# Kernel optimization log

Measured on AMD Instinct MI355X. Metric: run time of the kernel, lower is better.

Reference implementation:

```python
import jax, jax.numpy as jnp
import numpy as np

EMBED = 512
HEADS = 8
HEAD_DIM = EMBED // HEADS


def setup_inputs() -> dict:
    key = jax.random.key(0)
    ks = jax.random.split(key, 9)
    N, L = 4, 2048
    values = jax.random.normal(ks[0], (N, L, EMBED), dtype=jnp.float32)
    keys = jax.random.normal(ks[1], (N, L, EMBED), dtype=jnp.float32)
    query = jax.random.normal(ks[2], (N, L, EMBED), dtype=jnp.float32)
    mask = jax.random.randint(ks[3], (N, 1, 1, L), 0, 2, dtype=jnp.int32)
    s_h = 1.0 / np.sqrt(HEAD_DIM).astype(np.float32)
    s_e = 1.0 / np.sqrt(EMBED).astype(np.float32)
    Wv = jax.random.normal(ks[4], (HEAD_DIM, HEAD_DIM), dtype=jnp.float32) * s_h
    Wk = jax.random.normal(ks[5], (HEAD_DIM, HEAD_DIM), dtype=jnp.float32) * s_h
    Wq = jax.random.normal(ks[6], (HEAD_DIM, HEAD_DIM), dtype=jnp.float32) * s_h
    Wo = jax.random.normal(ks[7], (EMBED, EMBED), dtype=jnp.float32) * s_e
    bo = jnp.zeros((EMBED,), dtype=jnp.float32)
    return {"values": values, "keys": keys, "query": query, "mask": mask,
            "Wv": Wv, "Wk": Wk, "Wq": Wq, "Wo": Wo, "bo": bo}


def reference(values, keys, query, mask, Wv, Wk, Wq, Wo, bo):
    N, Lq, E = query.shape
    D = Wv.shape[0]
    H = E // D
    Lk = keys.shape[1]
    # split heads: [N, L, H, D]
    v = values.reshape(N, values.shape[1], H, D)
    k = keys.reshape(N, Lk, H, D)
    q = query.reshape(N, Lq, H, D)
    # per-head linear projections (nn.Linear: x @ W^T, no bias)
    v = jnp.einsum("nlhd,ed->nlhe", v, Wv)
    k = jnp.einsum("nlhd,ed->nlhe", k, Wk)
    q = jnp.einsum("nlhd,ed->nlhe", q, Wq)
    # energy: [N, H, Lq, Lk]
    energy = jnp.einsum("nqhd,nkhd->nhqk", q, k)
    energy = jnp.where(mask == 0, jnp.float32(-1e20), energy)
    # NOTE: original scales by sqrt(embed_size), not sqrt(head_dim)
    attn = jax.nn.softmax(energy / jnp.sqrt(jnp.float32(E)), axis=3)
    out = jnp.einsum("nhqk,nkhd->nqhd", attn, v).reshape(N, Lq, E)
    return out @ Wo.T + bo
```

## Files before the change

### kernel.cpp

```cpp
#include <hip/hip_runtime.h>

#define LSEQ 2048
#define EMB  512
#define NH   8
#define HD   64
#define NBATCH 4
#define QSCALE (0.044194173824159216f * 1.4426950408889634f)

using short8  = __attribute__((ext_vector_type(8))) short;
using short4v = __attribute__((ext_vector_type(4))) short;
using f32x4   = __attribute__((ext_vector_type(4))) float;

__device__ __forceinline__ short bf16r(float f) {
  union { float f; unsigned u; } x; x.f = f;
  unsigned r = x.u + 0x7FFFu + ((x.u >> 16) & 1u);
  return (short)(r >> 16);
}

__device__ __forceinline__ float exp2v(float x) {
  float r;
  asm("v_exp_f32 %0, %1" : "=v"(r) : "v"(x));
  return r;
}

__device__ __forceinline__ unsigned cvtpk(float lo, float hi) {
  unsigned r;
  asm("v_cvt_pk_bf16_f32 %0, %1, %2" : "=v"(r) : "v"(lo), "v"(hi));
  return r;
}

__device__ __forceinline__ void stage16(const void* g, void* l) {
  __builtin_amdgcn_global_load_lds(
      (const __attribute__((address_space(1))) unsigned int*)g,
      (__attribute__((address_space(3))) unsigned int*)l, 16, 0, 0);
}

__device__ __forceinline__ short8 cvt8(const float* __restrict__ p) {
  float4 a = ((const float4*)p)[0];
  float4 b = ((const float4*)p)[1];
  short8 r;
  r[0]=bf16r(a.x); r[1]=bf16r(a.y); r[2]=bf16r(a.z); r[3]=bf16r(a.w);
  r[4]=bf16r(b.x); r[5]=bf16r(b.y); r[6]=bf16r(b.z); r[7]=bf16r(b.w);
  return r;
}

__device__ __forceinline__ short8 ld8(const short* __restrict__ p) {
  return *(const short8*)p;
}

__global__ __launch_bounds__(256) void prep_kernel(
    const int* __restrict__ mask, float* __restrict__ fbias,
    int* __restrict__ kidx, int* __restrict__ meta,
    const float* __restrict__ Wq, const float* __restrict__ Wk,
    const float* __restrict__ Wv, short* __restrict__ Wqb,
    short* __restrict__ Wkb, short* __restrict__ Wvb) {
  __shared__ int ssum[256];
  int b = blockIdx.x;
  int tid = threadIdx.x;
  if (b < 4) {
    int n = b;
    int base = n * LSEQ;
    int loc[8], c = 0;
#pragma unroll
    for (int j = 0; j < 8; j++) { loc[j] = mask[base + tid * 8 + j] != 0; c += loc[j]; }
    ssum[tid] = c;
    __syncthreads();
    for (int off = 1; off < 256; off <<= 1) {
      int v = (tid >= off) ? ssum[tid - off] : 0;
      __syncthreads();
      ssum[tid] += v;
      __syncthreads();
    }
    int total = ssum[255];
    int excl = ssum[tid] - c;
    int qz = (total == 0);
#pragma unroll
    for (int j = 0; j < 8; j++) {
      int i = tid * 8 + j;
      kidx[base + i] = qz ? i : 0;
      fbias[base + i] = (qz || i < total) ? 0.f : -1e30f;
    }
    __syncthreads();
    if (!qz) {
      int pos = excl;
#pragma unroll
      for (int j = 0; j < 8; j++)
        if (loc[j]) { kidx[base + pos] = tid * 8 + j; pos++; }
    }
    if (tid == 0) {
      meta[n] = qz ? (LSEQ / 64) : ((total + 63) >> 6);
      meta[4 + n] = qz;
    }
  } else {
    int t = (b - 4) >> 2;
    int i = ((b - 4) & 3) * 256 + tid;
    const float* W = (t == 0) ? Wq : (t == 1) ? Wk : Wv;
    short* O = (t == 0) ? Wqb : (t == 1) ? Wkb : Wvb;
    float sc = (t == 0) ? QSCALE : 1.f;
    float4 v = ((const float4*)W)[i];
    short4v r;
    r[0]=bf16r(v.x*sc); r[1]=bf16r(v.y*sc); r[2]=bf16r(v.z*sc); r[3]=bf16r(v.w*sc);
    ((short4v*)O)[i] = r;
  }
}

__global__ __launch_bounds__(256) void proj_kernel(
    const float* __restrict__ keys, const float* __restrict__ values,
    const short* __restrict__ Wkb, const short* __restrict__ Wvb,
    const int* __restrict__ kidx, const int* __restrict__ meta,
    short* __restrict__ Kp, short* __restrict__ Vt) {
  __shared__ short tile[64][72];
  int t = blockIdx.y + 1;
  const float* x = (t == 1) ? keys : values;
  const short* W = (t == 1) ? Wkb  : Wvb;
  int idx = blockIdx.x;
  int lt = idx & 31, h = (idx >> 5) & 7, n = idx >> 8;
  int tid = threadIdx.x, lane = tid & 63, w = tid >> 6;
  int row16 = lane & 15, g = lane >> 4;
  int lbase = lt * 64 + w * 16;

  if (lbase >= ((meta[n] + 1) & ~1) * 64) return;
  int gidx = kidx[n * LSEQ + lbase + row16];
  const float* xr = x + ((size_t)(n * LSEQ + gidx)) * EMB + h * HD + g * 8;
  short8 a0 = cvt8(xr);
  short8 a1 = cvt8(xr + 32);

  f32x4 acc[4];
#pragma unroll
  for (int et = 0; et < 4; et++) acc[et] = (f32x4){0.f, 0.f, 0.f, 0.f};
#pragma unroll
  for (int et = 0; et < 4; et++) {
    const short* wr = W + (size_t)(et * 16 + row16) * HD + g * 8;
    short8 b0 = ld8(wr);
    short8 b1 = ld8(wr + 32);
    acc[et] = __builtin_amdgcn_mfma_f32_16x16x32_bf16(a0, b0, acc[et], 0, 0, 0);
    acc[et] = __builtin_amdgcn_mfma_f32_16x16x32_bf16(a1, b1, acc[et], 0, 0, 0);
  }

  if (t == 2) {
#pragma unroll
    for (int et = 0; et < 4; et++)
#pragma unroll
      for (int r = 0; r < 4; r++)
        tile[et * 16 + row16][w * 16 + g * 4 + r] = bf16r(acc[et][r]);
  } else {
#pragma unroll
    for (int et = 0; et < 4; et++)
#pragma unroll
      for (int r = 0; r < 4; r++)
        tile[w * 16 + g * 4 + r][et * 16 + row16] = bf16r(acc[et][r]);
  }
  __syncthreads();

  size_t nh = (size_t)(n * NH + h);
#pragma unroll
  for (int i = tid; i < 512; i += 256) {
    int rr = i >> 3, cc = i & 7;
    short8 v = *(const short8*)&tile[rr][cc * 8];
    if (t == 2)
      *(short8*)(Vt + (nh * HD + rr) * LSEQ + lt * 64 + cc * 8) = v;
    else
      *(short8*)(Kp + (nh * LSEQ + lt * 64 + rr) * HD + cc * 8) = v;
  }
}

__global__ __launch_bounds__(512, 4) void attn_kernel(
    const float* __restrict__ query, const short* __restrict__ Wqb,
    const short* __restrict__ Kp, const short* __restrict__ Vt,
    const float* __restrict__ fbias, const int* __restrict__ meta,
    short* __restrict__ aout, const float* __restrict__ Wo,
    short* __restrict__ Wob) {
  __shared__ __align__(16) char smem[49152];

  int idx = blockIdx.x;
  int tid = threadIdx.x;
  if (idx >= NBATCH * NH * (LSEQ / 128)) {
    int i = (idx - NBATCH * NH * (LSEQ / 128)) * 512 + tid;
    float4 v = ((const float4*)Wo)[i];
    short4v r;
    r[0]=bf16r(v.x); r[1]=bf16r(v.y); r[2]=bf16r(v.z); r[3]=bf16r(v.w);
    ((short4v*)Wob)[i] = r;
    return;
  }
  int h = idx & 7;
  int qt = (idx >> 3) & 15;
  int n = idx >> 7;
  int lane = tid & 63, w = tid >> 6;
  int q0 = lane & 15, g = lane >> 4;
  int xr = q0 & 7;
  int nkt = meta[n];

  size_t nh = (size_t)(n * NH + h);

  const char* Ksrc = (const char*)(Kp + nh * (size_t)LSEQ * HD);
  const char* Vsrc = (const char*)(Vt + nh * (size_t)HD * LSEQ);
  const float* fb  = fbias + n * LSEQ + g * 4;

  int c = w * 64 + lane;
  int rr_ = c >> 3, cw_ = (c & 7) ^ (rr_ & 7);
  int ksoff = rr_ * 128 + cw_ * 16;
  int vsoff = rr_ * (LSEQ * 2) + cw_ * 16;
  int ldo = (w * 64) * 16;

  int kfragb = q0 * 128 + ((g ^ xr) << 4);
  int pbase = 32768 + w * 2048 + q0 * 128;
  char* pw_[4];
#pragma unroll
  for (int ks = 0; ks < 4; ks++)
    pw_[ks] = smem + pbase + ((ks * 32 + g * 8) ^ (xr << 4));
  const char* pr0 = smem + pbase + ((g * 16) ^ (xr << 4));
  const char* pr1 = smem + pbase + ((64 + g * 16) ^ (xr << 4));

  stage16(Ksrc + ksoff, smem + ldo);
  stage16(Vsrc + vsoff, smem + 16384 + ldo);

  {
    short8 wf0[4], wf1[4];
#pragma unroll
    for (int et = 0; et < 4; et++) {
      wf0[et] = ld8(Wqb + (et * 16 + q0) * HD + g * 8);
      wf1[et] = ld8(Wqb + (et * 16 + q0) * HD + 32 + g * 8);
    }
    int zq = meta[4 + n];
    const float* xrow = query +
        ((size_t)(n * LSEQ + qt * 128 + w * 16 + q0)) * EMB + h * HD + g * 8;
    short8 xa0 = cvt8(xrow);
    short8 xa1 = cvt8(xrow + 32);
#pragma unroll
    for (int et = 0; et < 4; et++) {
      f32x4 tq = (f32x4){0.f, 0.f, 0.f, 0.f};
      tq = __builtin_amdgcn_mfma_f32_16x16x32_bf16(wf0[et], xa0, tq, 0, 0, 0);
      tq = __builtin_amdgcn_mfma_f32_16x16x32_bf16(wf1[et], xa1, tq, 0, 0, 0);
      if (zq) tq = (f32x4){0.f, 0.f, 0.f, 0.f};
      *(int2*)(smem + pbase + ((et * 32 + g * 8) ^ (xr << 4))) =
          make_int2((int)cvtpk(tq[0], tq[1]), (int)cvtpk(tq[2], tq[3]));
    }
  }
  asm volatile("s_waitcnt lgkmcnt(0)" ::: "memory");
  short8 bq0 = *(const short8*)pr0;
  short8 bq1 = *(const short8*)pr1;

  f32x4 acc[4];
#pragma unroll
  for (int dt = 0; dt < 4; dt++) acc[dt] = (f32x4){0.f, 0.f, 0.f, 0.f};
  float lsum = 0.f;

  __syncthreads();

  for (int kt = 0; kt < nkt; kt++) {
    int buf = kt & 1;
    if (kt < nkt - 1) {
      int bo = (buf ^ 1) * 8192;
      stage16(Ksrc + (size_t)(kt + 1) * 8192 + ksoff, smem + bo + ldo);
      stage16(Vsrc + (size_t)(kt + 1) * 128 + vsoff, smem + 16384 + bo + ldo);
    }
    f32x4 fbv[4];
#pragma unroll
    for (int ks = 0; ks < 4; ks++)
      fbv[ks] = *(const f32x4*)(fb + kt * 64 + ks * 16);

    int kb_l = buf * 8192 + kfragb;
    f32x4 s[4];
    __builtin_amdgcn_s_setprio(1);
#pragma unroll
    for (int ks = 0; ks < 4; ks++) {
      short8 k0 = *(const short8*)(smem + (kb_l + ks * 2048));
      short8 k1 = *(const short8*)(smem + ((kb_l + ks * 2048) ^ 64));
      f32x4 t = __builtin_amdgcn_mfma_f32_16x16x32_bf16(k0, bq0, fbv[ks], 0, 0, 0);
      s[ks]   = __builtin_amdgcn_mfma_f32_16x16x32_bf16(k1, bq1, t, 0, 0, 0);
    }
    __builtin_amdgcn_s_setprio(0);

    float ps = 0.f;
#pragma unroll
    for (int ks = 0; ks < 4; ks++) {
      float p0 = exp2v(s[ks][0] - 32.f), p1 = exp2v(s[ks][1] - 32.f);
      float p2 = exp2v(s[ks][2] - 32.f), p3 = exp2v(s[ks][3] - 32.f);
      ps += (p0 + p1) + (p2 + p3);
      *(int2*)pw_[ks] = make_int2((int)cvtpk(p0, p1), (int)cvtpk(p2, p3));
    }
    lsum += ps;

    asm volatile("s_waitcnt lgkmcnt(0)" ::: "memory");

    short8 ap0 = *(const short8*)pr0;
    short8 ap1 = *(const short8*)pr1;
    int vb_l = 16384 + buf * 8192 + kfragb;
    __builtin_amdgcn_s_setprio(1);
#pragma unroll
    for (int dt = 0; dt < 4; dt++) {
      short8 v0 = *(const short8*)(smem + (vb_l + dt * 2048));
      short8 v1 = *(const short8*)(smem + ((vb_l + dt * 2048) ^ 64));
      acc[dt] = __builtin_amdgcn_mfma_f32_16x16x32_bf16(ap0, v0, acc[dt], 0, 0, 0);
      acc[dt] = __builtin_amdgcn_mfma_f32_16x16x32_bf16(ap1, v1, acc[dt], 0, 0, 0);
    }
    __builtin_amdgcn_s_setprio(0);

    __syncthreads();
  }

  lsum += __shfl_xor(lsum, 16);
  lsum += __shfl_xor(lsum, 32);
  float linv = lsum > 0.f ? 1.f / lsum : 0.f;
  int lb = lane & 48;
  float li[4];
#pragma unroll
  for (int r = 0; r < 4; r++) li[r] = __shfl(linv, lb + g * 4 + r);

#pragma unroll
  for (int r = 0; r < 4; r++) {
    int q = qt * 128 + w * 16 + g * 4 + r;
#pragma unroll
    for (int dt = 0; dt < 4; dt++)
      aout[((size_t)(n * LSEQ + q)) * EMB + h * HD + dt * 16 + q0] =
          bf16r(acc[dt][r] * li[r]);
  }
}

__global__ __launch_bounds__(256) void outproj_kernel(
    const short* __restrict__ aout, const short* __restrict__ Wob,
    const float* __restrict__ bo, float* __restrict__ out) {
  int mt = blockIdx.x, nt = blockIdx.y;
  int tid = threadIdx.x, lane = tid & 63, w = tid >> 6;
  int row16 = lane & 15, g = lane >> 4;
  int mrow = mt * 256 + w * 64;

  f32x4 acc[4][4];
#pragma unroll
  for (int hh = 0; hh < 4; hh++)
#pragma unroll
    for (int et = 0; et < 4; et++) acc[hh][et] = (f32x4){0.f, 0.f, 0.f, 0.f};

  for (int kc = 0; kc < 16; kc++) {
    short8 a[4];
#pragma unroll
    for (int hh = 0; hh < 4; hh++)
      a[hh] = ld8(aout + (size_t)(mrow + hh * 16 + row16) * EMB + kc * 32 + g * 8);
#pragma unroll
    for (int et = 0; et < 4; et++) {
      short8 bw = ld8(Wob + (size_t)(nt * 64 + et * 16 + row16) * EMB + kc * 32 + g * 8);
#pragma unroll
      for (int hh = 0; hh < 4; hh++)
        acc[hh][et] = __builtin_amdgcn_mfma_f32_16x16x32_bf16(a[hh], bw, acc[hh][et], 0, 0, 0);
    }
  }
#pragma unroll
  for (int et = 0; et < 4; et++) {
    int e = nt * 64 + et * 16 + row16;
    float bias = bo[e];
#pragma unroll
    for (int hh = 0; hh < 4; hh++)
#pragma unroll
      for (int r = 0; r < 4; r++)
        out[(size_t)(mrow + hh * 16 + g * 4 + r) * EMB + e] = acc[hh][et][r] + bias;
  }
}

extern "C" void kernel_launch(void* const* d_in, const int* in_sizes, int n_in,
                              void* d_out, int out_size, void* d_ws, size_t ws_size,
                              hipStream_t stream) {
  const float* values = (const float*)d_in[0];
  const float* keys   = (const float*)d_in[1];
  const float* query  = (const float*)d_in[2];
  const int*   mask   = (const int*)d_in[3];
  const float* Wv     = (const float*)d_in[4];
  const float* Wk     = (const float*)d_in[5];
  const float* Wq     = (const float*)d_in[6];
  const float* Wo     = (const float*)d_in[7];
  const float* bo     = (const float*)d_in[8];
  float* out = (float*)d_out;

  short* Kp = (short*)d_out;
  char* ws = (char*)d_ws;
  short* Vt    = (short*)(ws);
  short* aout  = (short*)(ws + (8u << 20));
  short* Wob   = (short*)(ws + (16u << 20));
  float* fbias = (float*)(ws + (16u << 20) + (512u << 10));
  int*   kidx  = (int*)  (ws + (16u << 20) + (544u << 10));
  int*   meta  = (int*)  (ws + (16u << 20) + (576u << 10));
  short* Wqb   = (short*)(ws + (16u << 20) + (577u << 10));
  short* Wkb   = (short*)(ws + (16u << 20) + (585u << 10));
  short* Wvb   = (short*)(ws + (16u << 20) + (593u << 10));

  prep_kernel<<<16, 256, 0, stream>>>(mask, fbias, kidx, meta,
                                      Wq, Wk, Wv, Wqb, Wkb, Wvb);
  proj_kernel<<<dim3(NBATCH * NH * (LSEQ / 64), 2), 256, 0, stream>>>(
      keys, values, Wkb, Wvb, kidx, meta, Kp, Vt);
  attn_kernel<<<NBATCH * NH * (LSEQ / 128) + 128, 512, 0, stream>>>(
      query, Wqb, Kp, Vt, fbias, meta, aout, Wo, Wob);
  outproj_kernel<<<dim3((NBATCH * LSEQ) / 256, EMB / 64), 256, 0, stream>>>(
      aout, Wob, bo, out);
}
```

Before: 78.79 us.

## Triple-buffer K/V tiles with vmcnt waits and stage mask bias into LDS

Switches the K/V shared-memory staging from double to triple buffering, prefetching two tiles ahead. It waits on partial vmcnt counts before each barrier, so one tile's loads stay in flight across iterations. The per-key mask bias row is now staged once into LDS and read from there instead of from global memory every iteration. LDS use rises from 48KB to 72KB per block, which may lower occupancy against the launch bounds.

```diff
diff --git a/kernel.cpp b/kernel.cpp
--- a/kernel.cpp
+++ b/kernel.cpp
@@ -170,7 +170,7 @@
     const float* __restrict__ fbias, const int* __restrict__ meta,
     short* __restrict__ aout, const float* __restrict__ Wo,
     short* __restrict__ Wob) {
-  __shared__ __align__(16) char smem[49152];
+  __shared__ __align__(16) char smem[73728];
 
   int idx = blockIdx.x;
   int tid = threadIdx.x;
@@ -194,7 +194,6 @@
 
   const char* Ksrc = (const char*)(Kp + nh * (size_t)LSEQ * HD);
   const char* Vsrc = (const char*)(Vt + nh * (size_t)HD * LSEQ);
-  const float* fb  = fbias + n * LSEQ + g * 4;
 
   int c = w * 64 + lane;
   int rr_ = c >> 3, cw_ = (c & 7) ^ (rr_ & 7);
@@ -203,7 +202,7 @@
   int ldo = (w * 64) * 16;
 
   int kfragb = q0 * 128 + ((g ^ xr) << 4);
-  int pbase = 32768 + w * 2048 + q0 * 128;
+  int pbase = 49152 + w * 2048 + q0 * 128;
   char* pw_[4];
 #pragma unroll
   for (int ks = 0; ks < 4; ks++)
@@ -211,8 +210,13 @@
   const char* pr0 = smem + pbase + ((g * 16) ^ (xr << 4));
   const char* pr1 = smem + pbase + ((64 + g * 16) ^ (xr << 4));
 
+  stage16(fbias + n * LSEQ + w * 256 + lane * 4, smem + 65536 + w * 1024);
   stage16(Ksrc + ksoff, smem + ldo);
-  stage16(Vsrc + vsoff, smem + 16384 + ldo);
+  stage16(Vsrc + vsoff, smem + 8192 + ldo);
+  if (nkt > 1) {
+    stage16(Ksrc + 8192 + ksoff, smem + 16384 + ldo);
+    stage16(Vsrc + 128 + vsoff, smem + 16384 + 8192 + ldo);
+  }
 
   {
     short8 wf0[4], wf1[4];
@@ -245,21 +249,27 @@
   for (int dt = 0; dt < 4; dt++) acc[dt] = (f32x4){0.f, 0.f, 0.f, 0.f};
   float lsum = 0.f;
 
-  __syncthreads();
-
+  if (nkt > 1)
+    asm volatile("s_waitcnt vmcnt(2)" ::: "memory");
+  else
+    asm volatile("s_waitcnt vmcnt(0)" ::: "memory");
+  __builtin_amdgcn_sched_barrier(0);
+  __builtin_amdgcn_s_barrier();
+
+  int cb = 0, sb = 2;
   for (int kt = 0; kt < nkt; kt++) {
-    int buf = kt & 1;
-    if (kt < nkt - 1) {
-      int bo = (buf ^ 1) * 8192;
-      stage16(Ksrc + (size_t)(kt + 1) * 8192 + ksoff, smem + bo + ldo);
-      stage16(Vsrc + (size_t)(kt + 1) * 128 + vsoff, smem + 16384 + bo + ldo);
+    int bufo = cb * 16384;
+    if (kt + 2 < nkt) {
+      int sbo = sb * 16384;
+      stage16(Ksrc + (size_t)(kt + 2) * 8192 + ksoff, smem + sbo + ldo);
+      stage16(Vsrc + (size_t)(kt + 2) * 128 + vsoff, smem + sbo + 8192 + ldo);
     }
     f32x4 fbv[4];
 #pragma unroll
     for (int ks = 0; ks < 4; ks++)
-      fbv[ks] = *(const f32x4*)(fb + kt * 64 + ks * 16);
-
-    int kb_l = buf * 8192 + kfragb;
+      fbv[ks] = *(const f32x4*)(smem + 65536 + kt * 256 + ks * 64 + g * 16);
+
+    int kb_l = bufo + kfragb;
     f32x4 s[4];
     __builtin_amdgcn_s_setprio(1);
 #pragma unroll
@@ -285,7 +295,7 @@
 
     short8 ap0 = *(const short8*)pr0;
     short8 ap1 = *(const short8*)pr1;
-    int vb_l = 16384 + buf * 8192 + kfragb;
+    int vb_l = bufo + 8192 + kfragb;
     __builtin_amdgcn_s_setprio(1);
 #pragma unroll
     for (int dt = 0; dt < 4; dt++) {
@@ -296,7 +306,15 @@
     }
     __builtin_amdgcn_s_setprio(0);
 
-    __syncthreads();
+    if (kt + 2 < nkt)
+      asm volatile("s_waitcnt vmcnt(2)" ::: "memory");
+    else
+      asm volatile("s_waitcnt vmcnt(0)" ::: "memory");
+    __builtin_amdgcn_sched_barrier(0);
+    __builtin_amdgcn_s_barrier();
+
+    cb = (cb == 2) ? 0 : cb + 1;
+    sb = (sb == 2) ? 0 : sb + 1;
   }
 
   lsum += __shfl_xor(lsum, 16);
```

Measured after the change: 77.12 us. 1.02x faster.
